# Optimization experiments

Measured on AMD Instinct MI355X. Metric: run time of the kernel, lower is better.

The kernel has to match this reference:

```python
import jax, jax.numpy as jnp
import numpy as np

N_USER, N_ITEM, N_ENT = 60000, 30000, 15000
E_UI, E_IE = 1_000_000, 300_000
DIM, FACTOR_K, DIM_K, ITERS = 50, 2, 25, 4
INDEX = [(0, 1), (1, 0)] + [(1, j) for j in range(2, 8)]
I_LIST = [[0], [1, 2, 3, 4, 5, 6, 7]]


def _l2n(x):
    # F.normalize(p=2, dim=2), eps=1e-12
    return x / jnp.clip(jnp.linalg.norm(x, axis=2, keepdims=True), 1e-12)


def _forward(edges, embs_in, Wtk, at, W, q_rela):
    n_types = len(embs_in)
    # fac(): project each node type into factor_k subspaces [k, n, dim_k]
    embs = [_l2n(jax.nn.leaky_relu(jnp.einsum('nd,kde->kne', embs_in[i], Wtk[i]), 0.2))
            for i in range(n_types)]
    rows = [embs[a].shape[1] for (a, b) in INDEX]
    # r_rela init: uniform over factors, never fed back (as in the source)
    r_node = [jnp.full((FACTOR_K, rows[e]), 1.0 / FACTOR_K, dtype=embs[0].dtype)
              for e in range(len(INDEX))]

    def rela_update(edge, new_emb, old_emb, a, r_n, n_rows, q_r):
        u, col = edge[0], edge[1]
        # edge gather + attention score per factor: [k, E]
        ui = jnp.concatenate([new_emb[:, u], old_emb[:, col]], axis=2)  # [k,E,2*dk]
        e_ts_k = jax.nn.relu(jnp.einsum('ked,kd->ke', ui, a))
        vals = jnp.sum(e_ts_k * r_n[:, u], axis=0)  # [E]
        # sparse row-wise softmax (torch.sparse.softmax dim=1)
        m = jax.ops.segment_max(vals, u, num_segments=n_rows)
        ex = jnp.exp(vals - m[u])
        attn = ex / jax.ops.segment_sum(ex, u, num_segments=n_rows)[u]
        # sparse mm per factor: scatter attn-weighted neighbor features
        msg = attn[None, :, None] * old_emb[:, col]  # [k,E,dk]
        z = jax.vmap(lambda mk: jax.ops.segment_sum(mk, u, num_segments=n_rows))(msg)
        z = jnp.einsum('kne,ef->knf', jax.nn.leaky_relu(z, 0.2), W)
        r = jax.nn.softmax(jnp.einsum('kne,e->kn', jnp.tanh(z), q_r), axis=0)
        return r, z

    # note: in the source all_new_emb aliases all_ego_emb (same list), so updates persist
    for _ in range(ITERS):
        rl, el = [], []
        for e in range(len(INDEX)):
            a_i, b_i = INDEX[e]
            r, z = rela_update(edges[e], embs[a_i], embs[b_i], at[e], r_node[e], rows[e], q_rela[e])
            rl.append(r)
            el.append(z)
        for i in range(2):
            ego = embs[i]
            for j in I_LIST[i]:
                ego = ego + el[j] * rl[j][:, :, None]
            embs[i] = _l2n(ego)

    def flat(e):  # torch.cat(list(e), dim=1): [k,n,d] -> [n, k*d]
        k, n, d = e.shape
        return jnp.transpose(e, (1, 0, 2)).reshape(n, k * d)

    return jnp.concatenate([flat(embs[0]), flat(embs[1])], axis=0)


def setup_inputs() -> dict:
    key = jax.random.key(0)
    ks = jax.random.split(key, 40)
    inp = {}

    def edges(k1, k2, E, nr, nc):
        r = jax.random.randint(k1, (E,), 0, nr)
        c = jax.random.randint(k2, (E,), 0, nc)
        return jnp.stack([r, c]).astype(jnp.int32)

    inp['edge0'] = edges(ks[0], ks[1], E_UI, N_USER, N_ITEM)
    inp['edge1'] = edges(ks[2], ks[3], E_UI, N_ITEM, N_USER)
    for e in range(2, 8):
        inp[f'edge{e}'] = edges(ks[2 * e], ks[2 * e + 1], E_IE, N_ITEM, N_ENT)
    sizes = [N_USER, N_ITEM] + [N_ENT] * 6
    for i, n in enumerate(sizes):
        inp[f'emb{i}'] = jax.random.normal(ks[16 + i], (n, DIM), jnp.float32) * 0.1
    inp['Wtk'] = jax.random.normal(ks[30], (8, FACTOR_K, DIM, DIM_K), jnp.float32) * (2.0 / (DIM + DIM_K)) ** 0.5
    inp['at'] = jax.random.normal(ks[31], (8, FACTOR_K, 2 * DIM_K), jnp.float32) * 0.1
    inp['W'] = jax.random.normal(ks[32], (DIM_K, DIM_K), jnp.float32) * 0.2
    inp['q_rela'] = jax.random.normal(ks[33], (8, DIM_K), jnp.float32) * 0.2
    return inp


def reference(edge0, edge1, edge2, edge3, edge4, edge5, edge6, edge7,
              emb0, emb1, emb2, emb3, emb4, emb5, emb6, emb7,
              Wtk, at, W, q_rela):
    edges = [edge0, edge1, edge2, edge3, edge4, edge5, edge6, edge7]
    embs_in = [emb0, emb1, emb2, emb3, emb4, emb5, emb6, emb7]
    return _forward(edges, embs_in, Wtk, at, W, q_rela)
```

## Files before the change

kernel.cpp:

```cpp
#include <hip/hip_runtime.h>
#include <math.h>


#define KF 2
#define DK 25
#define DD 50
#define PS 52
#define ITERS 4
#define WPB 4

static __device__ __forceinline__ float leakyf(float x) { return x > 0.f ? x : 0.2f * x; }

static __device__ __forceinline__ float2 score_row50(const float* p, const float* a) {
    float s0 = 0.f, s1 = 0.f;
    #pragma unroll
    for (int f = 0; f < DK; ++f) {
        s0 = fmaf(p[f],      a[f],      s0);
        s1 = fmaf(p[DK + f], a[50 + f], s1);
    }
    return make_float2(s0, s1);
}
static __device__ __forceinline__ float2 score_col50(const float* p, const float* a) {
    float s0 = 0.f, s1 = 0.f;
    #pragma unroll
    for (int f = 0; f < DK; ++f) {
        s0 = fmaf(p[f],      a[25 + f], s0);
        s1 = fmaf(p[DK + f], a[75 + f], s1);
    }
    return make_float2(s0, s1);
}

struct FacArgs { const float* emb[8]; float* P[8]; const float* Wtk; int base[9]; };

__global__ void fac_kernel(FacArgs A) {
    int g = blockIdx.x * blockDim.x + threadIdx.x;
    if (g >= A.base[8]) return;
    int ty = 0;
    while (g >= A.base[ty + 1]) ++ty;
    int node = g - A.base[ty];
    const float* er = A.emb[ty] + (size_t)node * DD;
    const float* Wt = A.Wtk + (size_t)ty * KF * DD * DK;
    float x[DD];
    #pragma unroll
    for (int d = 0; d < DD; ++d) x[d] = er[d];
    float out[DD];
    #pragma unroll
    for (int k = 0; k < KF; ++k) {
        const float* Wk = Wt + k * DD * DK;
        float nrm = 0.f;
        for (int f = 0; f < DK; ++f) {
            float acc = 0.f;
            for (int d = 0; d < DD; ++d) acc = fmaf(x[d], Wk[d * DK + f], acc);
            acc = leakyf(acc);
            out[k * DK + f] = acc;
            nrm = fmaf(acc, acc, nrm);
        }
        float inv = 1.f / fmaxf(sqrtf(nrm), 1e-12f);
        for (int f = 0; f < DK; ++f) out[k * DK + f] *= inv;
    }
    float* Pr = A.P[ty] + (size_t)node * PS;
    #pragma unroll
    for (int j = 0; j < DD; ++j) Pr[j] = out[j];
    Pr[50] = 0.f; Pr[51] = 0.f;
}

struct EdgeArgs {
    const int* rows[8]; const int* cols[8];
    int* cnt;
    unsigned short* colind;
    int ebase[9];
    int rowbase[8];
};

__global__ void hist_kernel(EdgeArgs A) {
    int g = blockIdx.x * blockDim.x + threadIdx.x;
    if (g >= A.ebase[8]) return;
    int rel = 0;
    while (g >= A.ebase[rel + 1]) ++rel;
    int e = g - A.ebase[rel];
    atomicAdd(&A.cnt[A.rowbase[rel] + A.rows[rel][e]], 1);
}

__global__ __launch_bounds__(1024) void scan_part_kernel(int* a, int n, int* bsum) {
    __shared__ int lds[1024];
    int tid = threadIdx.x;
    int i = blockIdx.x * 1024 + tid;
    int v = (i < n) ? a[i] : 0;
    lds[tid] = v;
    __syncthreads();
    int x = v;
    for (int off = 1; off < 1024; off <<= 1) {
        int y = (tid >= off) ? lds[tid - off] : 0;
        __syncthreads();
        x += y;
        lds[tid] = x;
        __syncthreads();
    }
    if (i < n) a[i] = x - v;
    if (tid == 1023) bsum[blockIdx.x] = x;
}

__global__ __launch_bounds__(1024) void scan_bsum_kernel(int* bsum, int nb) {
    __shared__ int lds[1024];
    int tid = threadIdx.x;
    int v = (tid < nb) ? bsum[tid] : 0;
    lds[tid] = v;
    __syncthreads();
    int x = v;
    for (int off = 1; off < 1024; off <<= 1) {
        int y = (tid >= off) ? lds[tid - off] : 0;
        __syncthreads();
        x += y;
        lds[tid] = x;
        __syncthreads();
    }
    if (tid < nb) bsum[tid] = x - v;
}

__global__ __launch_bounds__(1024) void add_off_kernel(int* a, int n, const int* bsum) {
    int i = blockIdx.x * 1024 + threadIdx.x;
    if (i < n) a[i] += bsum[blockIdx.x];
}

__global__ void scatter_kernel(EdgeArgs A) {
    int g = blockIdx.x * blockDim.x + threadIdx.x;
    if (g >= A.ebase[8]) return;
    int rel = 0;
    while (g >= A.ebase[rel + 1]) ++rel;
    int e = g - A.ebase[rel];
    int p = atomicAdd(&A.cnt[A.rowbase[rel] + A.rows[rel][e]], 1);
    A.colind[p] = (unsigned short)A.cols[rel][e];
}

struct SbArgs { const float* Pb[6]; const float* at[6]; float2* sb[6]; int base[7]; };

__global__ void sb_kernel(SbArgs A) {
    int g = blockIdx.x * blockDim.x + threadIdx.x;
    if (g >= A.base[6]) return;
    int rel = 0;
    while (g >= A.base[rel + 1]) ++rel;
    int c = g - A.base[rel];
    const float* p = A.Pb[rel] + (size_t)c * PS;
    A.sb[rel][c] = score_col50(p, A.at[rel]);
}

struct ScoreArgs {
    const float* P0; const float* P1;
    const float* at;
    float2* sa[8]; float2* sb0; float2* sb1;
    int n0, n1;
};

__global__ void score01_kernel(ScoreArgs A) {
    int g = blockIdx.x * blockDim.x + threadIdx.x;
    if (g >= A.n0 + A.n1) return;
    if (g < A.n0) {
        const float* p = A.P0 + (size_t)g * PS;
        float pr[DD];
        #pragma unroll
        for (int j = 0; j < DD; ++j) pr[j] = p[j];
        A.sa[0][g] = score_row50(pr, A.at + 0);
        A.sb1[g]   = score_col50(pr, A.at + 100);
    } else {
        int node = g - A.n0;
        const float* p = A.P1 + (size_t)node * PS;
        float pr[DD];
        #pragma unroll
        for (int j = 0; j < DD; ++j) pr[j] = p[j];
        #pragma unroll
        for (int e = 1; e < 8; ++e) A.sa[e][node] = score_row50(pr, A.at + e * 100);
        A.sb0[node] = score_col50(pr, A.at + 0);
    }
}

struct PhaseArgs {
    const int* rowptr;
    const unsigned short* colind;
    const float* Pb[8];
    const float* q[8];
    const float2* sa[8]; const float2* sb[8];
    float* z[8]; float* r[8];
    const float* W;
    int rowbase[9];
};

__global__ __launch_bounds__(WPB * 64) void phase_kernel(PhaseArgs A, int totalRows) {
    int wave = blockIdx.x * WPB + (threadIdx.x >> 6);
    int lane = threadIdx.x & 63;
    if (wave >= totalRows) return;
    int rel = 0;
    while (wave >= A.rowbase[rel + 1]) ++rel;
    int u = wave - A.rowbase[rel];

    const unsigned short* colind = A.colind;
    const float* Pb = A.Pb[rel];
    const float* qv = A.q[rel];
    const float2* sb = A.sb[rel];
    float2 h = A.sa[rel][u];
    int beg = wave ? A.rowptr[wave - 1] : 0;
    int end = A.rowptr[wave];

    bool act = lane < DD;
    int grp4 = lane >> 4, sub4 = lane & 15;
    float ssum = 0.f;
    float4 a4 = make_float4(0.f, 0.f, 0.f, 0.f);

    for (int base = beg; base < end; base += 64) {
        int idx = base + lane;
        bool vld = idx < end;
        int cb = vld ? (int)colind[idx] : 0;
        float evl = 0.f;
        if (vld) {
            float2 sc = sb[cb];
            evl = __expf(0.5f * (fmaxf(h.x + sc.x, 0.f) + fmaxf(h.y + sc.y, 0.f)));
        }
        ssum += evl;
        int nb = min(64, end - base);
        #pragma unroll 2
        for (int t = 0; t < nb; t += 4) {
            int srcl = t + grp4;
            int c = __shfl(cb, srcl);
            float ev = __shfl(evl, srcl);
            const float4* pc = (const float4*)(Pb + (size_t)c * PS);
            float4 v = pc[sub4];
            a4.x = fmaf(ev, v.x, a4.x);
            a4.y = fmaf(ev, v.y, a4.y);
            a4.z = fmaf(ev, v.z, a4.z);
            a4.w = fmaf(ev, v.w, a4.w);
        }
    }
    #pragma unroll
    for (int off = 32; off >= 16; off >>= 1) {
        a4.x += __shfl_xor(a4.x, off);
        a4.y += __shfl_xor(a4.y, off);
        a4.z += __shfl_xor(a4.z, off);
        a4.w += __shfl_xor(a4.w, off);
    }
    #pragma unroll
    for (int off = 32; off; off >>= 1) ssum += __shfl_xor(ssum, off);

    int src = lane >> 2;
    float fx = __shfl(a4.x, src), fy = __shfl(a4.y, src);
    float fz = __shfl(a4.z, src), fw = __shfl(a4.w, src);
    float za = (lane & 1) ? ((lane & 2) ? fw : fy) : ((lane & 2) ? fz : fx);

    float inv = (ssum > 0.f) ? (1.f / ssum) : 0.f;
    float zl = act ? leakyf(za * inv) : 0.f;

    int fcol = act ? ((lane < DK) ? lane : (lane - DK)) : 0;
    int kbase = (act && lane >= DK) ? DK : 0;
    float o = 0.f;
    const float* W = A.W;
    #pragma unroll
    for (int d = 0; d < DK; ++d) {
        float zd = __shfl(zl, kbase + d);
        o = fmaf(zd, W[d * DK + fcol], o);
    }
    float th = act ? tanhf(o) * qv[fcol] : 0.f;
    float t0 = (lane < DK) ? th : 0.f;
    float t1 = th - t0;
    #pragma unroll
    for (int off = 32; off; off >>= 1) { t0 += __shfl_xor(t0, off); t1 += __shfl_xor(t1, off); }
    float m = fmaxf(t0, t1);
    float e0 = __expf(t0 - m), e1 = __expf(t1 - m);
    float rinv = 1.f / (e0 + e1);

    if (act) A.z[rel][(size_t)u * DD + lane] = o;
    if (lane == 0) {
        A.r[rel][(size_t)u * 2 + 0] = e0 * rinv;
        A.r[rel][(size_t)u * 2 + 1] = e1 * rinv;
    }
}

static __device__ __forceinline__ void l2norm_store(float* dst, const float* acc) {
    #pragma unroll
    for (int k = 0; k < KF; ++k) {
        float nrm = 0.f;
        for (int f = 0; f < DK; ++f) nrm = fmaf(acc[k * DK + f], acc[k * DK + f], nrm);
        float inv = 1.f / fmaxf(sqrtf(nrm), 1e-12f);
        for (int f = 0; f < DK; ++f) dst[k * DK + f] = acc[k * DK + f] * inv;
    }
}

struct EgoArgs { float* P0; float* P1; const float* zz[8]; const float* rr[8]; int n0, n1; };

__global__ void ego_kernel(EgoArgs A) {
    int g = blockIdx.x * blockDim.x + threadIdx.x;
    if (g >= A.n0 + A.n1) return;
    float acc[DD];
    if (g < A.n0) {
        float* Pr = A.P0 + (size_t)g * PS;
        const float* zr = A.zz[0] + (size_t)g * DD;
        float r0 = A.rr[0][(size_t)g * 2], r1 = A.rr[0][(size_t)g * 2 + 1];
        #pragma unroll
        for (int j = 0; j < DD; ++j) acc[j] = fmaf(zr[j], (j < DK ? r0 : r1), Pr[j]);
        l2norm_store(Pr, acc);
    } else {
        int node = g - A.n0;
        float* Pr = A.P1 + (size_t)node * PS;
        #pragma unroll
        for (int j = 0; j < DD; ++j) acc[j] = Pr[j];
        for (int e = 1; e < 8; ++e) {
            const float* zr = A.zz[e] + (size_t)node * DD;
            float r0 = A.rr[e][(size_t)node * 2], r1 = A.rr[e][(size_t)node * 2 + 1];
            #pragma unroll
            for (int j = 0; j < DD; ++j) acc[j] = fmaf(zr[j], (j < DK ? r0 : r1), acc[j]);
        }
        l2norm_store(Pr, acc);
    }
}

__global__ void out_kernel(const float* __restrict__ P0, const float* __restrict__ P1,
                           int n0, int n1, float* __restrict__ out) {
    int g = blockIdx.x * blockDim.x + threadIdx.x;
    if (g >= n0 + n1) return;
    const float* src = (g < n0) ? (P0 + (size_t)g * PS) : (P1 + (size_t)(g - n0) * PS);
    float* dst = out + (size_t)g * DD;
    #pragma unroll
    for (int j = 0; j < DD; ++j) dst[j] = src[j];
}

static inline int cdiv(int a, int b) { return (a + b - 1) / b; }

extern "C" void kernel_launch(void* const* d_in, const int* in_sizes, int n_in,
                              void* d_out, int out_size, void* d_ws, size_t ws_size,
                              hipStream_t stream) {
    const int* edge[8];
    int E[8];
    for (int e = 0; e < 8; ++e) { edge[e] = (const int*)d_in[e]; E[e] = in_sizes[e] / 2; }
    const float* emb[8];
    int nn[8];
    for (int i = 0; i < 8; ++i) { emb[i] = (const float*)d_in[8 + i]; nn[i] = in_sizes[8 + i] / DD; }
    const float* Wtk = (const float*)d_in[16];
    const float* at  = (const float*)d_in[17];
    const float* W   = (const float*)d_in[18];
    const float* q   = (const float*)d_in[19];
    float* out = (float*)d_out;

    static const int aIdx[8] = {0, 1, 1, 1, 1, 1, 1, 1};
    static const int bIdx[8] = {1, 0, 2, 3, 4, 5, 6, 7};
    int rows[8], ncol[8];
    for (int e = 0; e < 8; ++e) { rows[e] = nn[aIdx[e]]; ncol[e] = nn[bIdx[e]]; }
    int rowbase[9];
    rowbase[0] = 0;
    for (int e = 0; e < 8; ++e) rowbase[e + 1] = rowbase[e] + rows[e];
    int totalRows = rowbase[8];
    int ebase[9];
    ebase[0] = 0;
    for (int e = 0; e < 8; ++e) ebase[e + 1] = ebase[e] + E[e];
    int totE = ebase[8];

    char* w = (char*)d_ws;
    size_t off = 0;
    auto alloc_f  = [&](size_t n) { float*  p = (float*)(w + off);  off += n * 4; return p; };
    auto alloc_f2 = [&](size_t n) { float2* p = (float2*)(w + off); off += n * 8; return p; };
    auto alloc_i  = [&](size_t n) { int*    p = (int*)(w + off);    off += n * 4; return p; };
    float* P[8]; for (int i = 0; i < 8; ++i) P[i] = alloc_f((size_t)nn[i] * PS);
    float* z[8]; for (int e = 0; e < 8; ++e) z[e] = alloc_f((size_t)rows[e] * DD);
    float* r[8]; for (int e = 0; e < 8; ++e) r[e] = alloc_f((size_t)rows[e] * 2);
    float2* sb[8]; for (int e = 0; e < 8; ++e) sb[e] = alloc_f2((size_t)ncol[e]);
    float2* sa[8]; for (int e = 0; e < 8; ++e) sa[e] = alloc_f2((size_t)rows[e]);
    int* cnt = alloc_i((size_t)totalRows);
    int nchunks = cdiv(totalRows, 1024);
    int* bsum = alloc_i((size_t)nchunks);
    unsigned short* colind = (unsigned short*)(w + off);
    off += (size_t)totE * 2;
    (void)ws_size;

    const int B = 256;

    hipMemsetAsync(cnt, 0, (size_t)totalRows * 4, stream);
    EdgeArgs EA;
    for (int e = 0; e < 8; ++e) {
        EA.rows[e] = edge[e]; EA.cols[e] = edge[e] + E[e];
        EA.rowbase[e] = rowbase[e];
        EA.ebase[e] = ebase[e];
    }
    EA.ebase[8] = ebase[8];
    EA.cnt = cnt; EA.colind = colind;
    hist_kernel<<<cdiv(totE, B), B, 0, stream>>>(EA);
    scan_part_kernel<<<nchunks, 1024, 0, stream>>>(cnt, totalRows, bsum);
    scan_bsum_kernel<<<1, 1024, 0, stream>>>(bsum, nchunks);
    add_off_kernel<<<nchunks, 1024, 0, stream>>>(cnt, totalRows, bsum);
    scatter_kernel<<<cdiv(totE, B), B, 0, stream>>>(EA);

    FacArgs FA;
    FA.base[0] = 0;
    for (int i = 0; i < 8; ++i) { FA.emb[i] = emb[i]; FA.P[i] = P[i]; FA.base[i + 1] = FA.base[i] + nn[i]; }
    FA.Wtk = Wtk;
    fac_kernel<<<cdiv(FA.base[8], B), B, 0, stream>>>(FA);

    SbArgs SBs;
    SBs.base[0] = 0;
    for (int e = 2; e < 8; ++e) {
        SBs.Pb[e - 2] = P[bIdx[e]];
        SBs.at[e - 2] = at + (size_t)e * KF * DD;
        SBs.sb[e - 2] = sb[e];
        SBs.base[e - 1] = SBs.base[e - 2] + ncol[e];
    }
    sb_kernel<<<cdiv(SBs.base[6], B), B, 0, stream>>>(SBs);

    ScoreArgs SC;
    SC.P0 = P[0]; SC.P1 = P[1]; SC.at = at;
    for (int e = 0; e < 8; ++e) SC.sa[e] = sa[e];
    SC.sb0 = sb[0]; SC.sb1 = sb[1];
    SC.n0 = nn[0]; SC.n1 = nn[1];
    score01_kernel<<<cdiv(nn[0] + nn[1], B), B, 0, stream>>>(SC);

    PhaseArgs PA;
    PA.rowptr = cnt; PA.colind = colind;
    for (int e = 0; e < 8; ++e) {
        PA.Pb[e] = P[bIdx[e]];
        PA.q[e]  = q + (size_t)e * DK;
        PA.sa[e] = sa[e]; PA.sb[e] = sb[e];
        PA.z[e] = z[e]; PA.r[e] = r[e];
        PA.rowbase[e] = rowbase[e];
    }
    PA.rowbase[8] = rowbase[8];
    PA.W = W;
    EgoArgs GA;
    GA.P0 = P[0]; GA.P1 = P[1]; GA.n0 = nn[0]; GA.n1 = nn[1];
    for (int e = 0; e < 8; ++e) { GA.zz[e] = z[e]; GA.rr[e] = r[e]; }

    for (int it = 0; it < ITERS; ++it) {
        phase_kernel<<<cdiv(totalRows, WPB), WPB * 64, 0, stream>>>(PA, totalRows);
        ego_kernel<<<cdiv(nn[0] + nn[1], B), B, 0, stream>>>(GA);
        score01_kernel<<<cdiv(nn[0] + nn[1], B), B, 0, stream>>>(SC);
    }

    out_kernel<<<cdiv(nn[0] + nn[1], B), B, 0, stream>>>(P[0], P[1], nn[0], nn[1], out);
}
```

Before: 1.749 ms.

## Move W projection and factor softmax into fused ego+score kernel

The per-row W projection, tanh/q scoring and factor softmax leave the wave-per-row aggregation kernel, which now only writes the leaky-ReLU'd aggregate (padded to 52 floats). A new per-node ego kernel loads W into shared memory, does the projection, softmax and residual sum per relation, normalizes, and also computes the next iteration's attention scores. This removes the separate score kernel launch and the r buffer. The phase kernel also skips loads for idle lanes and uses a fast exp-based tanh. The risk is heavy per-thread register use in the ego kernel (several 50-float arrays), which could hurt occupancy.

```diff
diff --git a/kernel.cpp b/kernel.cpp
--- a/kernel.cpp
+++ b/kernel.cpp
@@ -10,6 +10,11 @@
 #define WPB 4
 
 static __device__ __forceinline__ float leakyf(float x) { return x > 0.f ? x : 0.2f * x; }
+
+static __device__ __forceinline__ float fast_tanhf(float x) {
+    float e = __expf(2.f * x);
+    return 1.f - 2.f * __builtin_amdgcn_rcpf(e + 1.f);
+}
 
 static __device__ __forceinline__ float2 score_row50(const float* p, const float* a) {
     float s0 = 0.f, s1 = 0.f;
@@ -177,10 +182,8 @@
     const int* rowptr;
     const unsigned short* colind;
     const float* Pb[8];
-    const float* q[8];
     const float2* sa[8]; const float2* sb[8];
-    float* z[8]; float* r[8];
-    const float* W;
+    float* z[8];
     int rowbase[9];
 };
 
@@ -194,14 +197,13 @@
 
     const unsigned short* colind = A.colind;
     const float* Pb = A.Pb[rel];
-    const float* qv = A.q[rel];
     const float2* sb = A.sb[rel];
     float2 h = A.sa[rel][u];
     int beg = wave ? A.rowptr[wave - 1] : 0;
     int end = A.rowptr[wave];
 
-    bool act = lane < DD;
     int grp4 = lane >> 4, sub4 = lane & 15;
+    bool ld = sub4 < 13;
     float ssum = 0.f;
     float4 a4 = make_float4(0.f, 0.f, 0.f, 0.f);
 
@@ -221,12 +223,14 @@
             int srcl = t + grp4;
             int c = __shfl(cb, srcl);
             float ev = __shfl(evl, srcl);
-            const float4* pc = (const float4*)(Pb + (size_t)c * PS);
-            float4 v = pc[sub4];
-            a4.x = fmaf(ev, v.x, a4.x);
-            a4.y = fmaf(ev, v.y, a4.y);
-            a4.z = fmaf(ev, v.z, a4.z);
-            a4.w = fmaf(ev, v.w, a4.w);
+            if (ld) {
+                const float4* pc = (const float4*)(Pb + (size_t)c * PS);
+                float4 v = pc[sub4];
+                a4.x = fmaf(ev, v.x, a4.x);
+                a4.y = fmaf(ev, v.y, a4.y);
+                a4.z = fmaf(ev, v.z, a4.z);
+                a4.w = fmaf(ev, v.w, a4.w);
+            }
         }
     }
     #pragma unroll
@@ -245,68 +249,96 @@
     float za = (lane & 1) ? ((lane & 2) ? fw : fy) : ((lane & 2) ? fz : fx);
 
     float inv = (ssum > 0.f) ? (1.f / ssum) : 0.f;
-    float zl = act ? leakyf(za * inv) : 0.f;
-
-    int fcol = act ? ((lane < DK) ? lane : (lane - DK)) : 0;
-    int kbase = (act && lane >= DK) ? DK : 0;
-    float o = 0.f;
-    const float* W = A.W;
-    #pragma unroll
-    for (int d = 0; d < DK; ++d) {
-        float zd = __shfl(zl, kbase + d);
-        o = fmaf(zd, W[d * DK + fcol], o);
-    }
-    float th = act ? tanhf(o) * qv[fcol] : 0.f;
-    float t0 = (lane < DK) ? th : 0.f;
-    float t1 = th - t0;
-    #pragma unroll
-    for (int off = 32; off; off >>= 1) { t0 += __shfl_xor(t0, off); t1 += __shfl_xor(t1, off); }
-    float m = fmaxf(t0, t1);
-    float e0 = __expf(t0 - m), e1 = __expf(t1 - m);
-    float rinv = 1.f / (e0 + e1);
-
-    if (act) A.z[rel][(size_t)u * DD + lane] = o;
-    if (lane == 0) {
-        A.r[rel][(size_t)u * 2 + 0] = e0 * rinv;
-        A.r[rel][(size_t)u * 2 + 1] = e1 * rinv;
-    }
-}
-
-static __device__ __forceinline__ void l2norm_store(float* dst, const float* acc) {
+    if (lane < DD) A.z[rel][(size_t)u * PS + lane] = leakyf(za * inv);
+}
+
+struct Ego2Args {
+    float* P0; float* P1;
+    const float* zz[8];
+    const float* W;
+    const float* q;
+    const float* at;
+    float2* sa[8]; float2* sb0; float2* sb1;
+    int n0, n1;
+};
+
+__global__ __launch_bounds__(256) void ego2_kernel(Ego2Args A) {
+    __shared__ float Ws[DK * DK];
+    for (int i = threadIdx.x; i < DK * DK; i += blockDim.x) Ws[i] = A.W[i];
+    __syncthreads();
+    int g = blockIdx.x * blockDim.x + threadIdx.x;
+    if (g >= A.n0 + A.n1) return;
+    bool is0 = g < A.n0;
+    int node = is0 ? g : g - A.n0;
+    float* Pr = (is0 ? A.P0 : A.P1) + (size_t)node * PS;
+
+    float acc[DD];
+    {
+        const float4* p4 = (const float4*)Pr;
+        #pragma unroll
+        for (int t = 0; t < 12; ++t) {
+            float4 v = p4[t];
+            acc[4 * t] = v.x; acc[4 * t + 1] = v.y; acc[4 * t + 2] = v.z; acc[4 * t + 3] = v.w;
+        }
+        acc[48] = Pr[48]; acc[49] = Pr[49];
+    }
+
+    int jbeg = is0 ? 0 : 1, jend = is0 ? 1 : 8;
+    for (int j = jbeg; j < jend; ++j) {
+        const float* zr = A.zz[j] + (size_t)node * PS;
+        float zl[DD];
+        {
+            const float4* z4 = (const float4*)zr;
+            #pragma unroll
+            for (int t = 0; t < 12; ++t) {
+                float4 v = z4[t];
+                zl[4 * t] = v.x; zl[4 * t + 1] = v.y; zl[4 * t + 2] = v.z; zl[4 * t + 3] = v.w;
+            }
+            zl[48] = zr[48]; zl[49] = zr[49];
+        }
+        const float* qv = A.q + (size_t)j * DK;
+        float o[DD];
+        float th[KF];
+        #pragma unroll
+        for (int k = 0; k < KF; ++k) {
+            float tsum = 0.f;
+            #pragma unroll
+            for (int f = 0; f < DK; ++f) {
+                float a = 0.f;
+                #pragma unroll
+                for (int d = 0; d < DK; ++d) a = fmaf(zl[k * DK + d], Ws[d * DK + f], a);
+                o[k * DK + f] = a;
+                tsum = fmaf(fast_tanhf(a), qv[f], tsum);
+            }
+            th[k] = tsum;
+        }
+        float m = fmaxf(th[0], th[1]);
+        float e0 = __expf(th[0] - m), e1 = __expf(th[1] - m);
+        float rinv = __builtin_amdgcn_rcpf(e0 + e1);
+        float r0 = e0 * rinv, r1 = e1 * rinv;
+        #pragma unroll
+        for (int f = 0; f < DD; ++f) acc[f] = fmaf(o[f], (f < DK) ? r0 : r1, acc[f]);
+    }
+
     #pragma unroll
     for (int k = 0; k < KF; ++k) {
         float nrm = 0.f;
+        #pragma unroll
         for (int f = 0; f < DK; ++f) nrm = fmaf(acc[k * DK + f], acc[k * DK + f], nrm);
         float inv = 1.f / fmaxf(sqrtf(nrm), 1e-12f);
-        for (int f = 0; f < DK; ++f) dst[k * DK + f] = acc[k * DK + f] * inv;
-    }
-}
-
-struct EgoArgs { float* P0; float* P1; const float* zz[8]; const float* rr[8]; int n0, n1; };
-
-__global__ void ego_kernel(EgoArgs A) {
-    int g = blockIdx.x * blockDim.x + threadIdx.x;
-    if (g >= A.n0 + A.n1) return;
-    float acc[DD];
-    if (g < A.n0) {
-        float* Pr = A.P0 + (size_t)g * PS;
-        const float* zr = A.zz[0] + (size_t)g * DD;
-        float r0 = A.rr[0][(size_t)g * 2], r1 = A.rr[0][(size_t)g * 2 + 1];
-        #pragma unroll
-        for (int j = 0; j < DD; ++j) acc[j] = fmaf(zr[j], (j < DK ? r0 : r1), Pr[j]);
-        l2norm_store(Pr, acc);
+        #pragma unroll
+        for (int f = 0; f < DK; ++f) acc[k * DK + f] *= inv;
+    }
+    #pragma unroll
+    for (int f = 0; f < DD; ++f) Pr[f] = acc[f];
+
+    if (is0) {
+        A.sa[0][node] = score_row50(acc, A.at + 0);
+        A.sb1[node]   = score_col50(acc, A.at + 100);
     } else {
-        int node = g - A.n0;
-        float* Pr = A.P1 + (size_t)node * PS;
-        #pragma unroll
-        for (int j = 0; j < DD; ++j) acc[j] = Pr[j];
-        for (int e = 1; e < 8; ++e) {
-            const float* zr = A.zz[e] + (size_t)node * DD;
-            float r0 = A.rr[e][(size_t)node * 2], r1 = A.rr[e][(size_t)node * 2 + 1];
-            #pragma unroll
-            for (int j = 0; j < DD; ++j) acc[j] = fmaf(zr[j], (j < DK ? r0 : r1), acc[j]);
-        }
-        l2norm_store(Pr, acc);
+        #pragma unroll
+        for (int e = 1; e < 8; ++e) A.sa[e][node] = score_row50(acc, A.at + e * 100);
+        A.sb0[node] = score_col50(acc, A.at + 0);
     }
 }
 
@@ -356,8 +388,7 @@
     auto alloc_f2 = [&](size_t n) { float2* p = (float2*)(w + off); off += n * 8; return p; };
     auto alloc_i  = [&](size_t n) { int*    p = (int*)(w + off);    off += n * 4; return p; };
     float* P[8]; for (int i = 0; i < 8; ++i) P[i] = alloc_f((size_t)nn[i] * PS);
-    float* z[8]; for (int e = 0; e < 8; ++e) z[e] = alloc_f((size_t)rows[e] * DD);
-    float* r[8]; for (int e = 0; e < 8; ++e) r[e] = alloc_f((size_t)rows[e] * 2);
+    float* z[8]; for (int e = 0; e < 8; ++e) z[e] = alloc_f((size_t)rows[e] * PS);
     float2* sb[8]; for (int e = 0; e < 8; ++e) sb[e] = alloc_f2((size_t)ncol[e]);
     float2* sa[8]; for (int e = 0; e < 8; ++e) sa[e] = alloc_f2((size_t)rows[e]);
     int* cnt = alloc_i((size_t)totalRows);
@@ -411,21 +442,21 @@
     PA.rowptr = cnt; PA.colind = colind;
     for (int e = 0; e < 8; ++e) {
         PA.Pb[e] = P[bIdx[e]];
-        PA.q[e]  = q + (size_t)e * DK;
         PA.sa[e] = sa[e]; PA.sb[e] = sb[e];
-        PA.z[e] = z[e]; PA.r[e] = r[e];
+        PA.z[e] = z[e];
         PA.rowbase[e] = rowbase[e];
     }
     PA.rowbase[8] = rowbase[8];
-    PA.W = W;
-    EgoArgs GA;
-    GA.P0 = P[0]; GA.P1 = P[1]; GA.n0 = nn[0]; GA.n1 = nn[1];
-    for (int e = 0; e < 8; ++e) { GA.zz[e] = z[e]; GA.rr[e] = r[e]; }
+
+    Ego2Args G2;
+    G2.P0 = P[0]; G2.P1 = P[1]; G2.n0 = nn[0]; G2.n1 = nn[1];
+    for (int e = 0; e < 8; ++e) { G2.zz[e] = z[e]; G2.sa[e] = sa[e]; }
+    G2.W = W; G2.q = q; G2.at = at;
+    G2.sb0 = sb[0]; G2.sb1 = sb[1];
 
     for (int it = 0; it < ITERS; ++it) {
         phase_kernel<<<cdiv(totalRows, WPB), WPB * 64, 0, stream>>>(PA, totalRows);
-        ego_kernel<<<cdiv(nn[0] + nn[1], B), B, 0, stream>>>(GA);
-        score01_kernel<<<cdiv(nn[0] + nn[1], B), B, 0, stream>>>(SC);
+        ego2_kernel<<<cdiv(nn[0] + nn[1], B), B, 0, stream>>>(G2);
     }
 
     out_kernel<<<cdiv(nn[0] + nn[1], B), B, 0, stream>>>(P[0], P[1], nn[0], nn[1], out);
```

Measured after the change: 5.894 ms. +237.0%, slower.
